# Kernel optimization log

Hardware: AMD Instinct MI355X
Metric: run time of the kernel (lower is better)

## Reference

```python
import jax, jax.numpy as jnp
import numpy as np

N = 100_000      # total nodes (entities + relations)
D = 128          # embed_dim
E_ER = 1_000_000 # entity->relation edges
E_EE = 500_000   # entity->entity edges


def setup_inputs() -> dict:
    key = jax.random.key(0)
    ks = jax.random.split(key, 14)
    s = 0.05
    return {
        "node_emb": jax.random.normal(ks[0], (N, D), jnp.float32),
        "er_src": jax.random.randint(ks[1], (E_ER,), 0, N),
        "er_dst": jax.random.randint(ks[2], (E_ER,), 0, N),
        "ee_src": jax.random.randint(ks[3], (E_EE,), 0, N),
        "ee_dst": jax.random.randint(ks[4], (E_EE,), 0, N),
        "ee_weight": jax.random.uniform(ks[5], (E_EE,), jnp.float32),
        # learned params (stored as (in, out) so y = x @ W + b)
        "W_attn_w": jax.random.normal(ks[6], (2 * D, D), jnp.float32) * s,
        "W_attn_b": jax.random.normal(ks[7], (D,), jnp.float32) * s,
        "w0_w": jax.random.normal(ks[8], (D,), jnp.float32) * s,
        "w0_b": jax.random.normal(ks[9], (), jnp.float32) * s,
        "W_self_w": jax.random.normal(ks[10], (D, D), jnp.float32) * s,
        "W_self_b": jax.random.normal(ks[11], (D,), jnp.float32) * s,
        "W_neigh_w": jax.random.normal(ks[12], (D, D), jnp.float32) * s,
        "W_neigh_b": jax.random.normal(ks[13], (D,), jnp.float32) * s,
    }


def _segment_softmax(values, seg_ids, num_segments):
    # torch scatter_reduce_ starts from zeros with include_self=True -> max includes 0
    seg_max = jnp.maximum(
        jax.ops.segment_max(values, seg_ids, num_segments=num_segments), 0.0)
    exp_v = jnp.exp(values - seg_max[seg_ids])
    seg_sum = jax.ops.segment_sum(exp_v, seg_ids, num_segments=num_segments)
    return exp_v / (seg_sum[seg_ids] + 1e-9)


def reference(node_emb, er_src, er_dst, ee_src, ee_dst, ee_weight,
              W_attn_w, W_attn_b, w0_w, w0_b, W_self_w, W_self_b,
              W_neigh_w, W_neigh_b):
    n = node_emb.shape[0]
    # --- entity -> relation attention messages ---
    h_emb = node_emb[er_src]                      # (E, D)
    r_emb = node_emb[er_dst]                      # (E, D)
    pair = jnp.concatenate([r_emb, h_emb], axis=-1)  # (E, 2D)
    e_ij = jnp.tanh(pair @ W_attn_w + W_attn_b) @ w0_w + w0_b  # (E,)
    attn = _segment_softmax(e_ij, er_src, n)      # (E,)
    r_msg = r_emb @ W_neigh_w + W_neigh_b         # (E, D)
    agg = jnp.zeros_like(node_emb).at[er_src].add(attn[:, None] * r_msg)
    # --- entity -> entity weighted messages (note: scatter index is ee_src, as in source) ---
    src_emb = node_emb[ee_src]                    # (E2, D)
    ee_msg = src_emb @ W_neigh_w + W_neigh_b
    agg = agg.at[ee_src].add(ee_weight[:, None] * ee_msg)
    # --- self update ---
    return jnp.tanh(node_emb @ W_self_w + W_self_b + agg)
```

## Files before the change

kernel.cpp:

```cpp
#include <hip/hip_runtime.h>

#define DD 128

typedef short s16x8 __attribute__((ext_vector_type(8)));
typedef float f32x4 __attribute__((ext_vector_type(4)));

__device__ __forceinline__ float tanh_fast(float x) {
  float e = __expf(2.0f * x);
  float r = __builtin_amdgcn_rcpf(e + 1.0f);
  return fmaf(-2.0f, r, 1.0f);
}

__device__ __forceinline__ unsigned short f2bf(float f) {
  unsigned u = __float_as_uint(f);
  u += 0x7FFFu + ((u >> 16) & 1u);
  return (unsigned short)(u >> 16);
}

__device__ __forceinline__ float bf2f(unsigned short u) {
  return __uint_as_float(((unsigned)u) << 16);
}

__device__ __forceinline__ float bfu(unsigned w, int odd) {
  return __uint_as_float(odd ? (w & 0xFFFF0000u) : (w << 16));
}

extern "C" __global__ __launch_bounds__(256) void k_misc(
    const float* __restrict__ Wattn, unsigned short* __restrict__ WB,
    const float* __restrict__ Wself, const float* __restrict__ Wneigh,
    unsigned short* __restrict__ WBh, unsigned short* __restrict__ WBl,
    const int* __restrict__ er_src, int* __restrict__ count, int nER, int hb,
    const int* __restrict__ ee_src, const float* __restrict__ ee_w,
    float* __restrict__ g, int nEE) {
  const int b = blockIdx.x;
  const int tid = threadIdx.x;
  if (b < 16) {
    int t = b * 256 + tid;
    int lane = t & 63;
    int cks = t >> 6;
    int ks = cks & 3, ct = cks >> 2;
    int c = ct * 16 + (lane & 15);
    int kb = ks * 32 + ((lane >> 4) << 3);
    const float* srcp = (c < DD) ? (Wattn + (size_t)kb * DD + c)
                                 : (Wattn + (size_t)(DD + kb) * DD + (c - DD));
    unsigned short* dst = WB + (size_t)t * 8;
#pragma unroll
    for (int j = 0; j < 8; ++j) dst[j] = f2bf(srcp[(size_t)j * DD]);
  } else if (b < 32) {
    int t = (b - 16) * 256 + tid;
    int lane = t & 63;
    int cks = t >> 6;
    int ks = cks & 7, ct = cks >> 3;
    int c = ct * 16 + (lane & 15);
    int k0 = ks * 32 + ((lane >> 4) << 3);
#pragma unroll
    for (int j = 0; j < 8; ++j) {
      int k = k0 + j;
      float v = (k < DD) ? Wself[(size_t)k * DD + c]
                         : Wneigh[(size_t)(k - DD) * DD + c];
      unsigned short h = f2bf(v);
      float r = v - bf2f(h);
      WBh[(size_t)t * 8 + j] = h;
      WBl[(size_t)t * 8 + j] = f2bf(r);
    }
  } else if (b < 32 + hb) {
    int e = (b - 32) * 256 + tid;
    if (e < nER) atomicAdd(&count[er_src[e]], 1);
  } else {
    int e = (b - 32 - hb) * 256 + tid;
    if (e < nEE) unsafeAtomicAdd(&g[ee_src[e]], ee_w[e]);
  }
}

extern "C" __global__ __launch_bounds__(256) void k_pq_mfma(
    const float* __restrict__ emb, const unsigned short* __restrict__ WB,
    const float* __restrict__ battn, unsigned short* __restrict__ PQE, int n) {
  const int wave = threadIdx.x >> 6, lane = threadIdx.x & 63;
  const int v0 = blockIdx.x * 64 + wave * 16;
  const int row = v0 + (lane & 15);
  const int kb = (lane >> 4) << 3;
  const bool rok = row < n;
  s16x8 a[4];
#pragma unroll
  for (int ks = 0; ks < 4; ++ks) {
    unsigned short tmp[8] = {0, 0, 0, 0, 0, 0, 0, 0};
    if (rok) {
      float4 xa = *(const float4*)(emb + (size_t)row * DD + ks * 32 + kb);
      float4 xb = *(const float4*)(emb + (size_t)row * DD + ks * 32 + kb + 4);
      tmp[0] = f2bf(xa.x); tmp[1] = f2bf(xa.y);
      tmp[2] = f2bf(xa.z); tmp[3] = f2bf(xa.w);
      tmp[4] = f2bf(xb.x); tmp[5] = f2bf(xb.y);
      tmp[6] = f2bf(xb.z); tmp[7] = f2bf(xb.w);
    }
    a[ks] = *(const s16x8*)tmp;
    if (rok)
      *(s16x8*)(PQE + (size_t)row * 384 + 128 + ks * 32 + kb) = a[ks];
  }
  f32x4 acc[16];
#pragma unroll
  for (int ct = 0; ct < 16; ++ct) acc[ct] = (f32x4)(0.f);
  const s16x8* wb = (const s16x8*)WB;
#pragma unroll
  for (int ct = 0; ct < 16; ++ct) {
#pragma unroll
    for (int ks = 0; ks < 4; ++ks) {
      s16x8 b = wb[(ct * 4 + ks) * 64 + lane];
      acc[ct] = __builtin_amdgcn_mfma_f32_16x16x32_bf16(a[ks], b, acc[ct], 0, 0, 0);
    }
  }
  const int r0 = (lane >> 4) << 2;
  const int col0 = lane & 15;
#pragma unroll
  for (int ct = 0; ct < 16; ++ct) {
    int c = ct * 16 + col0;
    float bias = (c < DD) ? battn[c] : 0.f;
    int dsto = (c < DD) ? c : (c - DD + 256);
#pragma unroll
    for (int r = 0; r < 4; ++r) {
      int v = v0 + r0 + r;
      if (v < n) PQE[(size_t)v * 384 + dsto] = f2bf(acc[ct][r] + bias);
    }
  }
}

extern "C" __global__ __launch_bounds__(256) void k_scan(
    const int* __restrict__ in, int* __restrict__ outp,
    int* __restrict__ bsum, int n) {
  __shared__ int s[512];
  __shared__ int total;
  const int t = threadIdx.x;
  const int base = blockIdx.x * 512;
  for (int i = t; i < 512; i += 256) s[i] = (base + i < n) ? in[base + i] : 0;
  __syncthreads();
  for (int d = 1; d < 512; d <<= 1) {
    int stride = d * 2;
    int nidx = 512 / stride;
    if (t < nidx) {
      int idx = (t + 1) * stride - 1;
      s[idx] += s[idx - d];
    }
    __syncthreads();
  }
  if (t == 0) { total = s[511]; s[511] = 0; }
  __syncthreads();
  for (int d = 256; d >= 1; d >>= 1) {
    int stride = d * 2;
    int nidx = 512 / stride;
    if (t < nidx) {
      int idx = (t + 1) * stride - 1;
      int tmp = s[idx - d];
      s[idx - d] = s[idx];
      s[idx] += tmp;
    }
    __syncthreads();
  }
  for (int i = t; i < 512; i += 256)
    if (base + i < n) outp[base + i] = s[i];
  if (t == 0) bsum[blockIdx.x] = total;
}

extern "C" __global__ __launch_bounds__(256) void k_scan_add(
    int* __restrict__ off, int* __restrict__ off_mut,
    const int* __restrict__ bofs, int n, int total) {
  int base = blockIdx.x * 512;
  int add = bofs[blockIdx.x];
  for (int i = threadIdx.x; i < 512; i += 256) {
    int idx = base + i;
    if (idx < n) {
      int val = off[idx] + add;
      off[idx] = val;
      off_mut[idx] = val;
    }
  }
  if (blockIdx.x == 0 && threadIdx.x == 0) off[n] = total;
}

extern "C" __global__ __launch_bounds__(256) void k_scatter_dst(
    const int* __restrict__ src, const int* __restrict__ dstp,
    int* __restrict__ off_mut, int* __restrict__ dst_s, int nE) {
  int e = blockIdx.x * 256 + threadIdx.x;
  if (e >= nE) return;
  int pos = atomicAdd(&off_mut[src[e]], 1);
  dst_s[pos] = dstp[e];
}

extern "C" __global__ __launch_bounds__(256) void k_fused(
    const unsigned short* __restrict__ PQE, const int* __restrict__ off,
    const int* __restrict__ dst_s, const float* __restrict__ w0w,
    const float* __restrict__ w0b, float* __restrict__ U,
    float* __restrict__ ssum, int n) {
  int v = (blockIdx.x * 256 + threadIdx.x) >> 6;
  int lane = threadIdx.x & 63;
  if (v >= n) return;
  const int l16 = lane & 15;
  const int grp = lane >> 4;
  const int start = off[v], end = off[v + 1];
  const float K = 2.8853900817779268f;
  float q2[8], w[8];
  {
    uint4 qv = *(const uint4*)(PQE + (size_t)v * 384 + 256 + l16 * 8);
    unsigned qq[4] = {qv.x, qv.y, qv.z, qv.w};
    float4 wa = *(const float4*)&w0w[l16 * 8];
    float4 wc = *(const float4*)&w0w[l16 * 8 + 4];
    w[0] = wa.x; w[1] = wa.y; w[2] = wa.z; w[3] = wa.w;
    w[4] = wc.x; w[5] = wc.y; w[6] = wc.z; w[7] = wc.w;
#pragma unroll
    for (int j = 0; j < 8; ++j) q2[j] = K * bfu(qq[j >> 1], j & 1);
  }
  const float wb = w0b[0];
  float a[8] = {0.f, 0.f, 0.f, 0.f, 0.f, 0.f, 0.f, 0.f};
  float ssv = 0.f;
  int i = start + grp;
  uint4 pv, ev;
  if (i < end) {
    const unsigned short* pe = PQE + (size_t)dst_s[i] * 384 + l16 * 8;
    pv = *(const uint4*)pe;
    ev = *(const uint4*)(pe + 128);
  }
  while (i < end) {
    int inx = i + 4;
    uint4 pvn, evn;
    if (inx < end) {
      const unsigned short* pen = PQE + (size_t)dst_s[inx] * 384 + l16 * 8;
      pvn = *(const uint4*)pen;
      evn = *(const uint4*)(pen + 128);
    }
    unsigned pw[4] = {pv.x, pv.y, pv.z, pv.w};
    unsigned ew[4] = {ev.x, ev.y, ev.z, ev.w};
    float part = 0.f;
#pragma unroll
    for (int j = 0; j < 8; ++j) {
      float x = bfu(pw[j >> 1], j & 1);
      float e = exp2f(fmaf(x, K, q2[j]));
      float r = __builtin_amdgcn_rcpf(e + 1.0f);
      float t = fmaf(-2.0f, r, 1.0f);
      part = fmaf(t, w[j], part);
    }
    part += __shfl_xor(part, 8);
    part += __shfl_xor(part, 4);
    part += __shfl_xor(part, 2);
    part += __shfl_xor(part, 1);
    float p = __expf(part + wb);
    ssv += p;
#pragma unroll
    for (int j = 0; j < 8; ++j)
      a[j] = fmaf(p, bfu(ew[j >> 1], j & 1), a[j]);
    i = inx;
    pv = pvn;
    ev = evn;
  }
#pragma unroll
  for (int j = 0; j < 8; ++j) {
    a[j] += __shfl_xor(a[j], 16);
    a[j] += __shfl_xor(a[j], 32);
  }
  ssv += __shfl_xor(ssv, 16);
  ssv += __shfl_xor(ssv, 32);
  if (grp == 0) {
    float4 o0 = make_float4(a[0], a[1], a[2], a[3]);
    float4 o1 = make_float4(a[4], a[5], a[6], a[7]);
    *(float4*)(U + (size_t)v * DD + l16 * 8) = o0;
    *(float4*)(U + (size_t)v * DD + l16 * 8 + 4) = o1;
    if (l16 == 0) ssum[v] = ssv;
  }
}

extern "C" __global__ __launch_bounds__(256) void k_out_mfma(
    const float* __restrict__ emb, const float* __restrict__ U,
    const float* __restrict__ ssum, const float* __restrict__ g,
    const unsigned short* __restrict__ WBh, const unsigned short* __restrict__ WBl,
    const float* __restrict__ bself, const float* __restrict__ bneigh,
    float* __restrict__ out, int n) {
  const int wave = threadIdx.x >> 6, lane = threadIdx.x & 63;
  const int v0 = blockIdx.x * 64 + wave * 16;
  const int row = v0 + (lane & 15);
  const int kb = (lane >> 4) << 3;
  const bool rok = row < n;
  float inv = 0.f, gv = 0.f;
  if (rok) {
    float sv = ssum[row];
    inv = 1.f / (sv + 1e-9f);
    gv = g[row];
  }
  s16x8 ah[8], al[8];
#pragma unroll
  for (int ks = 0; ks < 8; ++ks) {
    int k0 = (ks & 3) * 32 + kb;
    float x[8] = {0.f, 0.f, 0.f, 0.f, 0.f, 0.f, 0.f, 0.f};
    if (rok) {
      float4 ea = *(const float4*)(emb + (size_t)row * DD + k0);
      float4 eb = *(const float4*)(emb + (size_t)row * DD + k0 + 4);
      x[0] = ea.x; x[1] = ea.y; x[2] = ea.z; x[3] = ea.w;
      x[4] = eb.x; x[5] = eb.y; x[6] = eb.z; x[7] = eb.w;
      if (ks >= 4) {
        float4 ua = *(const float4*)(U + (size_t)row * DD + k0);
        float4 ub = *(const float4*)(U + (size_t)row * DD + k0 + 4);
        x[0] = fmaf(gv, x[0], ua.x * inv);
        x[1] = fmaf(gv, x[1], ua.y * inv);
        x[2] = fmaf(gv, x[2], ua.z * inv);
        x[3] = fmaf(gv, x[3], ua.w * inv);
        x[4] = fmaf(gv, x[4], ub.x * inv);
        x[5] = fmaf(gv, x[5], ub.y * inv);
        x[6] = fmaf(gv, x[6], ub.z * inv);
        x[7] = fmaf(gv, x[7], ub.w * inv);
      }
    }
    unsigned short hh[8], ll[8];
#pragma unroll
    for (int j = 0; j < 8; ++j) {
      unsigned short h = f2bf(x[j]);
      hh[j] = h;
      ll[j] = f2bf(x[j] - bf2f(h));
    }
    ah[ks] = *(const s16x8*)hh;
    al[ks] = *(const s16x8*)ll;
  }
  f32x4 acc[8];
#pragma unroll
  for (int ct = 0; ct < 8; ++ct) acc[ct] = (f32x4)(0.f);
  const s16x8* wbh = (const s16x8*)WBh;
  const s16x8* wbl = (const s16x8*)WBl;
#pragma unroll
  for (int ct = 0; ct < 8; ++ct) {
#pragma unroll
    for (int ks = 0; ks < 8; ++ks) {
      s16x8 bh = wbh[(ct * 8 + ks) * 64 + lane];
      s16x8 bl = wbl[(ct * 8 + ks) * 64 + lane];
      acc[ct] = __builtin_amdgcn_mfma_f32_16x16x32_bf16(ah[ks], bh, acc[ct], 0, 0, 0);
      acc[ct] = __builtin_amdgcn_mfma_f32_16x16x32_bf16(al[ks], bh, acc[ct], 0, 0, 0);
      acc[ct] = __builtin_amdgcn_mfma_f32_16x16x32_bf16(ah[ks], bl, acc[ct], 0, 0, 0);
    }
  }
  const int r0 = (lane >> 4) << 2;
  const int col0 = lane & 15;
  float tgr[4];
#pragma unroll
  for (int r = 0; r < 4; ++r) {
    int v = v0 + r0 + r;
    float tg = 0.f;
    if (v < n) {
      float sv = ssum[v];
      tg = sv / (sv + 1e-9f) + g[v];
    }
    tgr[r] = tg;
  }
#pragma unroll
  for (int ct = 0; ct < 8; ++ct) {
    int c = ct * 16 + col0;
    float bs = bself[c], bn = bneigh[c];
#pragma unroll
    for (int r = 0; r < 4; ++r) {
      int v = v0 + r0 + r;
      if (v < n) out[(size_t)v * DD + c] = tanh_fast(acc[ct][r] + bs + tgr[r] * bn);
    }
  }
}

static inline size_t al16(size_t x) { return (x + 15) & ~(size_t)15; }

extern "C" void kernel_launch(void* const* d_in, const int* in_sizes, int n_in,
                              void* d_out, int out_size, void* d_ws, size_t ws_size,
                              hipStream_t stream) {
  const float* emb = (const float*)d_in[0];
  const int* er_src = (const int*)d_in[1];
  const int* er_dst = (const int*)d_in[2];
  const int* ee_src = (const int*)d_in[3];
  const float* ee_w = (const float*)d_in[5];
  const float* Wattn = (const float*)d_in[6];
  const float* battn = (const float*)d_in[7];
  const float* w0w = (const float*)d_in[8];
  const float* w0b = (const float*)d_in[9];
  const float* Wself = (const float*)d_in[10];
  const float* bself = (const float*)d_in[11];
  const float* Wneigh = (const float*)d_in[12];
  const float* bneigh = (const float*)d_in[13];
  const int n = in_sizes[0] / DD;
  const int nER = in_sizes[1];
  const int nEE = in_sizes[3];

  char* w = (char*)d_ws;
  size_t o = 0;
  unsigned short* PQE = (unsigned short*)(w + o); o += al16((size_t)n * 384 * 2);
  float* U = (float*)(w + o);   o += al16((size_t)n * DD * 4);
  int* dst_s = (int*)(w + o);   o += al16((size_t)nER * 4);
  int* count = (int*)(w + o);   o += al16((size_t)n * 4);
  float* g = (float*)(w + o);   o += al16((size_t)n * 4);
  int* off = (int*)(w + o);     o += al16((size_t)(n + 4) * 4);
  int* off_mut = (int*)(w + o); o += al16((size_t)n * 4);
  float* ssum = (float*)(w + o); o += al16((size_t)n * 4);
  unsigned short* WB = (unsigned short*)(w + o);   o += 65536;
  unsigned short* WB2h = (unsigned short*)(w + o); o += 65536;
  unsigned short* WB2l = (unsigned short*)(w + o); o += 65536;
  int* bsum = (int*)(w + o);    o += 4096;
  int* dummy = (int*)(w + o);   o += 64;

  const int nb = (n + 511) / 512;
  const int hb = (nER + 255) / 256;
  const int db = (nEE + 255) / 256;

  hipMemsetAsync(count, 0, (size_t)n * 8, stream);

  k_misc<<<32 + hb + db, 256, 0, stream>>>(Wattn, WB, Wself, Wneigh, WB2h, WB2l,
                                           er_src, count, nER, hb, ee_src, ee_w,
                                           g, nEE);
  k_pq_mfma<<<(n + 63) / 64, 256, 0, stream>>>(emb, WB, battn, PQE, n);
  k_scan<<<nb, 256, 0, stream>>>(count, off, bsum, n);
  k_scan<<<1, 256, 0, stream>>>(bsum, bsum, dummy, nb);
  k_scan_add<<<nb, 256, 0, stream>>>(off, off_mut, bsum, n, nER);
  k_scatter_dst<<<(nER + 255) / 256, 256, 0, stream>>>(er_src, er_dst, off_mut,
                                                       dst_s, nER);
  k_fused<<<(n + 3) / 4, 256, 0, stream>>>(PQE, off, dst_s, w0w, w0b,
                                           U, ssum, n);
  k_out_mfma<<<(n + 63) / 64, 256, 0, stream>>>(emb, U, ssum, g, WB2h, WB2l,
                                                bself, bneigh, (float*)d_out, n);
}
```

Measured before the change: 349.1 us.

## Fuse attention aggregation with output MFMA kernel via shared-memory staging

Merges the per-node attention gather kernel and the output GEMM kernel into one kernel. Each wave now processes its 16 nodes one after another and keeps the aggregated message rows and softmax sums in LDS, so the global U and ssum buffers and one kernel launch go away. The cost is less parallelism: each wave runs a serial chain of gather loops, and the block's roughly 33KB of LDS may limit how many blocks fit per CU, which reduces latency hiding for the irregular gathers.

```diff
diff --git a/kernel.cpp b/kernel.cpp
--- a/kernel.cpp
+++ b/kernel.cpp
@@ -184,101 +184,104 @@
   dst_s[pos] = dstp[e];
 }
 
-extern "C" __global__ __launch_bounds__(256) void k_fused(
+extern "C" __global__ __launch_bounds__(256) void k_fused_out(
     const unsigned short* __restrict__ PQE, const int* __restrict__ off,
     const int* __restrict__ dst_s, const float* __restrict__ w0w,
-    const float* __restrict__ w0b, float* __restrict__ U,
-    float* __restrict__ ssum, int n) {
-  int v = (blockIdx.x * 256 + threadIdx.x) >> 6;
-  int lane = threadIdx.x & 63;
-  if (v >= n) return;
+    const float* __restrict__ w0b, const float* __restrict__ emb,
+    const float* __restrict__ g, const unsigned short* __restrict__ WBh,
+    const unsigned short* __restrict__ WBl, const float* __restrict__ bself,
+    const float* __restrict__ bneigh, float* __restrict__ out, int n) {
+  __shared__ float Us[64][132];
+  __shared__ float ssb[64];
+  const int wave = threadIdx.x >> 6, lane = threadIdx.x & 63;
   const int l16 = lane & 15;
   const int grp = lane >> 4;
-  const int start = off[v], end = off[v + 1];
+  const int vbase = blockIdx.x * 64 + wave * 16;
   const float K = 2.8853900817779268f;
-  float q2[8], w[8];
+  float w[8];
   {
-    uint4 qv = *(const uint4*)(PQE + (size_t)v * 384 + 256 + l16 * 8);
-    unsigned qq[4] = {qv.x, qv.y, qv.z, qv.w};
     float4 wa = *(const float4*)&w0w[l16 * 8];
     float4 wc = *(const float4*)&w0w[l16 * 8 + 4];
     w[0] = wa.x; w[1] = wa.y; w[2] = wa.z; w[3] = wa.w;
     w[4] = wc.x; w[5] = wc.y; w[6] = wc.z; w[7] = wc.w;
-#pragma unroll
-    for (int j = 0; j < 8; ++j) q2[j] = K * bfu(qq[j >> 1], j & 1);
   }
   const float wb = w0b[0];
-  float a[8] = {0.f, 0.f, 0.f, 0.f, 0.f, 0.f, 0.f, 0.f};
-  float ssv = 0.f;
-  int i = start + grp;
-  uint4 pv, ev;
-  if (i < end) {
-    const unsigned short* pe = PQE + (size_t)dst_s[i] * 384 + l16 * 8;
-    pv = *(const uint4*)pe;
-    ev = *(const uint4*)(pe + 128);
-  }
-  while (i < end) {
-    int inx = i + 4;
-    uint4 pvn, evn;
-    if (inx < end) {
-      const unsigned short* pen = PQE + (size_t)dst_s[inx] * 384 + l16 * 8;
-      pvn = *(const uint4*)pen;
-      evn = *(const uint4*)(pen + 128);
-    }
-    unsigned pw[4] = {pv.x, pv.y, pv.z, pv.w};
-    unsigned ew[4] = {ev.x, ev.y, ev.z, ev.w};
-    float part = 0.f;
+
+#pragma unroll 1
+  for (int t = 0; t < 16; ++t) {
+    int v = vbase + t;
+    if (v >= n) break;
+    const int start = off[v], end = off[v + 1];
+    float q2[8];
+    {
+      uint4 qv = *(const uint4*)(PQE + (size_t)v * 384 + 256 + l16 * 8);
+      unsigned qq[4] = {qv.x, qv.y, qv.z, qv.w};
+#pragma unroll
+      for (int j = 0; j < 8; ++j) q2[j] = K * bfu(qq[j >> 1], j & 1);
+    }
+    float a[8] = {0.f, 0.f, 0.f, 0.f, 0.f, 0.f, 0.f, 0.f};
+    float ssv = 0.f;
+    int i = start + grp;
+    uint4 pv, ev;
+    if (i < end) {
+      const unsigned short* pe = PQE + (size_t)dst_s[i] * 384 + l16 * 8;
+      pv = *(const uint4*)pe;
+      ev = *(const uint4*)(pe + 128);
+    }
+    while (i < end) {
+      int inx = i + 4;
+      uint4 pvn, evn;
+      if (inx < end) {
+        const unsigned short* pen = PQE + (size_t)dst_s[inx] * 384 + l16 * 8;
+        pvn = *(const uint4*)pen;
+        evn = *(const uint4*)(pen + 128);
+      }
+      unsigned pw[4] = {pv.x, pv.y, pv.z, pv.w};
+      unsigned ew[4] = {ev.x, ev.y, ev.z, ev.w};
+      float part = 0.f;
+#pragma unroll
+      for (int j = 0; j < 8; ++j) {
+        float x = bfu(pw[j >> 1], j & 1);
+        float e = exp2f(fmaf(x, K, q2[j]));
+        float r = __builtin_amdgcn_rcpf(e + 1.0f);
+        float tt = fmaf(-2.0f, r, 1.0f);
+        part = fmaf(tt, w[j], part);
+      }
+      part += __shfl_xor(part, 8);
+      part += __shfl_xor(part, 4);
+      part += __shfl_xor(part, 2);
+      part += __shfl_xor(part, 1);
+      float p = __expf(part + wb);
+      ssv += p;
+#pragma unroll
+      for (int j = 0; j < 8; ++j)
+        a[j] = fmaf(p, bfu(ew[j >> 1], j & 1), a[j]);
+      i = inx;
+      pv = pvn;
+      ev = evn;
+    }
 #pragma unroll
     for (int j = 0; j < 8; ++j) {
-      float x = bfu(pw[j >> 1], j & 1);
-      float e = exp2f(fmaf(x, K, q2[j]));
-      float r = __builtin_amdgcn_rcpf(e + 1.0f);
-      float t = fmaf(-2.0f, r, 1.0f);
-      part = fmaf(t, w[j], part);
-    }
-    part += __shfl_xor(part, 8);
-    part += __shfl_xor(part, 4);
-    part += __shfl_xor(part, 2);
-    part += __shfl_xor(part, 1);
-    float p = __expf(part + wb);
-    ssv += p;
-#pragma unroll
-    for (int j = 0; j < 8; ++j)
-      a[j] = fmaf(p, bfu(ew[j >> 1], j & 1), a[j]);
-    i = inx;
-    pv = pvn;
-    ev = evn;
-  }
-#pragma unroll
-  for (int j = 0; j < 8; ++j) {
-    a[j] += __shfl_xor(a[j], 16);
-    a[j] += __shfl_xor(a[j], 32);
-  }
-  ssv += __shfl_xor(ssv, 16);
-  ssv += __shfl_xor(ssv, 32);
-  if (grp == 0) {
-    float4 o0 = make_float4(a[0], a[1], a[2], a[3]);
-    float4 o1 = make_float4(a[4], a[5], a[6], a[7]);
-    *(float4*)(U + (size_t)v * DD + l16 * 8) = o0;
-    *(float4*)(U + (size_t)v * DD + l16 * 8 + 4) = o1;
-    if (l16 == 0) ssum[v] = ssv;
-  }
-}
-
-extern "C" __global__ __launch_bounds__(256) void k_out_mfma(
-    const float* __restrict__ emb, const float* __restrict__ U,
-    const float* __restrict__ ssum, const float* __restrict__ g,
-    const unsigned short* __restrict__ WBh, const unsigned short* __restrict__ WBl,
-    const float* __restrict__ bself, const float* __restrict__ bneigh,
-    float* __restrict__ out, int n) {
-  const int wave = threadIdx.x >> 6, lane = threadIdx.x & 63;
-  const int v0 = blockIdx.x * 64 + wave * 16;
-  const int row = v0 + (lane & 15);
-  const int kb = (lane >> 4) << 3;
+      a[j] += __shfl_xor(a[j], 16);
+      a[j] += __shfl_xor(a[j], 32);
+    }
+    ssv += __shfl_xor(ssv, 16);
+    ssv += __shfl_xor(ssv, 32);
+    if (grp == 0) {
+      int lr = wave * 16 + t;
+      *(float4*)&Us[lr][l16 * 8] = make_float4(a[0], a[1], a[2], a[3]);
+      *(float4*)&Us[lr][l16 * 8 + 4] = make_float4(a[4], a[5], a[6], a[7]);
+      if (l16 == 0) ssb[lr] = ssv;
+    }
+  }
+
+  const int row = vbase + l16;
+  const int lrow = wave * 16 + l16;
+  const int kb = (grp) << 3;
   const bool rok = row < n;
   float inv = 0.f, gv = 0.f;
   if (rok) {
-    float sv = ssum[row];
+    float sv = ssb[lrow];
     inv = 1.f / (sv + 1e-9f);
     gv = g[row];
   }
@@ -293,8 +296,8 @@
       x[0] = ea.x; x[1] = ea.y; x[2] = ea.z; x[3] = ea.w;
       x[4] = eb.x; x[5] = eb.y; x[6] = eb.z; x[7] = eb.w;
       if (ks >= 4) {
-        float4 ua = *(const float4*)(U + (size_t)row * DD + k0);
-        float4 ub = *(const float4*)(U + (size_t)row * DD + k0 + 4);
+        float4 ua = *(const float4*)&Us[lrow][k0];
+        float4 ub = *(const float4*)&Us[lrow][k0 + 4];
         x[0] = fmaf(gv, x[0], ua.x * inv);
         x[1] = fmaf(gv, x[1], ua.y * inv);
         x[2] = fmaf(gv, x[2], ua.z * inv);
@@ -331,26 +334,25 @@
       acc[ct] = __builtin_amdgcn_mfma_f32_16x16x32_bf16(ah[ks], bl, acc[ct], 0, 0, 0);
     }
   }
-  const int r0 = (lane >> 4) << 2;
-  const int col0 = lane & 15;
+  const int r0 = grp << 2;
   float tgr[4];
 #pragma unroll
   for (int r = 0; r < 4; ++r) {
-    int v = v0 + r0 + r;
+    int v = vbase + r0 + r;
     float tg = 0.f;
     if (v < n) {
-      float sv = ssum[v];
+      float sv = ssb[wave * 16 + r0 + r];
       tg = sv / (sv + 1e-9f) + g[v];
     }
     tgr[r] = tg;
   }
 #pragma unroll
   for (int ct = 0; ct < 8; ++ct) {
-    int c = ct * 16 + col0;
+    int c = ct * 16 + l16;
     float bs = bself[c], bn = bneigh[c];
 #pragma unroll
     for (int r = 0; r < 4; ++r) {
-      int v = v0 + r0 + r;
+      int v = vbase + r0 + r;
       if (v < n) out[(size_t)v * DD + c] = tanh_fast(acc[ct][r] + bs + tgr[r] * bn);
     }
   }
@@ -381,13 +383,11 @@
   char* w = (char*)d_ws;
   size_t o = 0;
   unsigned short* PQE = (unsigned short*)(w + o); o += al16((size_t)n * 384 * 2);
-  float* U = (float*)(w + o);   o += al16((size_t)n * DD * 4);
   int* dst_s = (int*)(w + o);   o += al16((size_t)nER * 4);
   int* count = (int*)(w + o);   o += al16((size_t)n * 4);
   float* g = (float*)(w + o);   o += al16((size_t)n * 4);
   int* off = (int*)(w + o);     o += al16((size_t)(n + 4) * 4);
   int* off_mut = (int*)(w + o); o += al16((size_t)n * 4);
-  float* ssum = (float*)(w + o); o += al16((size_t)n * 4);
   unsigned short* WB = (unsigned short*)(w + o);   o += 65536;
   unsigned short* WB2h = (unsigned short*)(w + o); o += 65536;
   unsigned short* WB2l = (unsigned short*)(w + o); o += 65536;
@@ -409,8 +409,7 @@
   k_scan_add<<<nb, 256, 0, stream>>>(off, off_mut, bsum, n, nER);
   k_scatter_dst<<<(nER + 255) / 256, 256, 0, stream>>>(er_src, er_dst, off_mut,
                                                        dst_s, nER);
-  k_fused<<<(n + 3) / 4, 256, 0, stream>>>(PQE, off, dst_s, w0w, w0b,
-                                           U, ssum, n);
-  k_out_mfma<<<(n + 63) / 64, 256, 0, stream>>>(emb, U, ssum, g, WB2h, WB2l,
-                                                bself, bneigh, (float*)d_out, n);
-}
+  k_fused_out<<<(n + 63) / 64, 256, 0, stream>>>(PQE, off, dst_s, w0w, w0b,
+                                                 emb, g, WB2h, WB2l, bself,
+                                                 bneigh, (float*)d_out, n);
+}
```

Result: slower. 421.1 us (+20.6%).
